# Optimization experiments

Hardware: AMD Instinct MI355X
Metric: run time of the kernel (lower is better)

## Reference

```python
import jax, jax.numpy as jnp
import numpy as np
from jax import lax

K_NN = 20          # cfg.nsample
BN_EPS = 1e-5


def fps(xyz, npoint, farthest0):
    """Furthest point sampling. xyz: [B,N,3] -> idx [B,npoint] (int)."""
    B, N, _ = xyz.shape

    def step(carry, _):
        distance, far = carry                                  # [B,N], [B]
        centroid = jnp.take_along_axis(xyz, far[:, None, None], axis=1)  # [B,1,3]
        d = jnp.sum((xyz - centroid) ** 2, axis=-1)            # [B,N]
        distance = jnp.minimum(distance, d)
        new_far = jnp.argmax(distance, axis=-1)
        return (distance, new_far), far

    init = (jnp.full((B, N), 1e10, dtype=xyz.dtype), farthest0)
    (_, _), idxs = lax.scan(step, init, None, length=npoint)   # idxs: [npoint,B]
    return jnp.transpose(idxs)                                 # [B,npoint]


def setup_inputs() -> dict:
    key = jax.random.key(0)
    k1, k2, k3, k4 = jax.random.split(key, 4)
    B, N, C = 4, 8192, 128
    c_in = C * 2 + 6   # mlps[0]*2 + 6 (use_xyz) = 262
    c_out = 256
    xyz = jax.random.normal(k1, (B, N, 3), dtype=jnp.float32)
    feat = jax.random.normal(k2, (B, N, C), dtype=jnp.float32)
    conv_w = jax.random.normal(k3, (c_in, c_out), dtype=jnp.float32) * 0.05  # 1x1 conv
    bn_gamma = jnp.ones((c_out,), dtype=jnp.float32)
    bn_beta = jnp.zeros((c_out,), dtype=jnp.float32)
    init_farthest = jax.random.randint(k4, (B,), 0, N)
    return {"xyz": xyz, "feat": feat, "conv_w": conv_w, "bn_gamma": bn_gamma,
            "bn_beta": bn_beta, "init_farthest": init_farthest, "npoints": 2048}


def reference(xyz, feat, conv_w, bn_gamma, bn_beta, init_farthest, npoints):
    # --- FPS sampling ---
    sample_idx = fps(xyz, npoints, init_farthest)                      # [B,S]
    new_xyz = jnp.take_along_axis(xyz, sample_idx[:, :, None], axis=1)  # [B,S,3]

    # --- augment features with xyz (use_xyz=True) ---
    feat_aug = jnp.concatenate([feat, xyz], axis=-1)                   # [B,N,131]
    new_feat_aug = jnp.take_along_axis(feat_aug, sample_idx[:, :, None], axis=1)  # [B,S,131]

    # --- KNN of new_xyz in xyz (squared L2, ascending) ---
    d2 = (jnp.sum(new_xyz ** 2, -1)[:, :, None]
          - 2.0 * jnp.einsum('bsd,bnd->bsn', new_xyz, xyz)
          + jnp.sum(xyz ** 2, -1)[:, None, :])                         # [B,S,N]
    _, knn_idx = lax.top_k(-d2, K_NN)                                  # [B,S,K]

    # --- gather neighbor features, build edge features ---
    knn_feat = jax.vmap(lambda f, i: f[i])(feat_aug, knn_idx)          # [B,S,K,131]
    center = new_feat_aug[:, :, None, :]                               # [B,S,1,131]
    edge = jnp.concatenate(
        [knn_feat - center, jnp.broadcast_to(center, knn_feat.shape)], axis=-1)  # [B,S,K,262]

    # --- shared MLP: 1x1 conv + BN (batch stats) + ReLU ---
    h = jnp.einsum('bskc,co->bsko', edge, conv_w)                      # [B,S,K,256]
    mean = jnp.mean(h, axis=(0, 1, 2))
    var = jnp.var(h, axis=(0, 1, 2))
    h = (h - mean) * lax.rsqrt(var + BN_EPS) * bn_gamma + bn_beta
    h = jax.nn.relu(h)

    # --- max-pool over K neighbors ---
    new_feat = jnp.max(h, axis=2)                                      # [B,S,256]
    return (new_xyz, new_feat, sample_idx)
```

## Files before the change

### kernel.cpp

```cpp
#include <hip/hip_runtime.h>
#include <hip/hip_bf16.h>


#define NPTS   8192
#define NSAMP  2048
#define KNN    20

typedef unsigned long long u64;
typedef unsigned int u32;
typedef unsigned short u16;

template<int CTRL, int RM>
__device__ __forceinline__ u64 dpp_kmax(u64 k) {
  unsigned lo = (unsigned)k, hi = (unsigned)(k >> 32);
  unsigned lo2 = (unsigned)__builtin_amdgcn_update_dpp((int)lo, (int)lo, CTRL, RM, 0xf, false);
  unsigned hi2 = (unsigned)__builtin_amdgcn_update_dpp((int)hi, (int)hi, CTRL, RM, 0xf, false);
  u64 o = ((u64)hi2 << 32) | lo2;
  return o > k ? o : k;
}
template<int CTRL, int RM>
__device__ __forceinline__ u64 dpp_kmin(u64 k) {
  unsigned lo = (unsigned)k, hi = (unsigned)(k >> 32);
  unsigned lo2 = (unsigned)__builtin_amdgcn_update_dpp((int)lo, (int)lo, CTRL, RM, 0xf, false);
  unsigned hi2 = (unsigned)__builtin_amdgcn_update_dpp((int)hi, (int)hi, CTRL, RM, 0xf, false);
  u64 o = ((u64)hi2 << 32) | lo2;
  return o < k ? o : k;
}
__device__ __forceinline__ u64 umax64(u64 a, u64 b) { return a > b ? a : b; }

__device__ __forceinline__ unsigned mspread4(unsigned q) {
  return (q & 1u) | ((q & 2u) << 2) | ((q & 4u) << 4) | ((q & 8u) << 6);
}

__global__ __launch_bounds__(1024, 1) void fps_kernel(
    const float* __restrict__ xyz, const int* __restrict__ farthest0,
    int* __restrict__ sample_int, float* __restrict__ out) {
  __shared__ float sxyz[NPTS * 3];
  __shared__ u16   sidxr[NPTS];
  __shared__ u32   s_samp[NSAMP];
  __shared__ u32   hist[4096];
  __shared__ u32   part[1024];
  __shared__ u64   slot[3];
  __shared__ int   s_isp;
  const int b = blockIdx.x, tid = threadIdx.x, lane = tid & 63;
  const float* xb = xyz + (size_t)b * NPTS * 3;

  for (int i = tid; i < 4096; i += 1024) hist[i] = 0u;
  if (tid < 3) slot[tid] = 0ull;
  __syncthreads();

  float ox[8], oy[8], oz[8];
  int cell[8];
#pragma unroll
  for (int j = 0; j < 8; ++j) {
    int p = tid * 8 + j;
    float x = xb[3*p], y = xb[3*p+1], z = xb[3*p+2];
    ox[j] = x; oy[j] = y; oz[j] = z;
    unsigned qx = (unsigned)(int)fminf(fmaxf((x + 5.2f) * 1.5384615f, 0.f), 15.f);
    unsigned qy = (unsigned)(int)fminf(fmaxf((y + 5.2f) * 1.5384615f, 0.f), 15.f);
    unsigned qz = (unsigned)(int)fminf(fmaxf((z + 5.2f) * 1.5384615f, 0.f), 15.f);
    cell[j] = (int)(mspread4(qx) | (mspread4(qy) << 1) | (mspread4(qz) << 2));
    atomicAdd(&hist[cell[j]], 1u);
  }
  __syncthreads();

  u32 h0 = hist[4*tid], h1 = hist[4*tid+1], h2 = hist[4*tid+2], h3 = hist[4*tid+3];
  u32 mysum = h0 + h1 + h2 + h3;
  part[tid] = mysum;
  __syncthreads();
  for (int off = 1; off < 1024; off <<= 1) {
    u32 u = (tid >= off) ? part[tid - off] : 0u;
    u32 v = part[tid];
    __syncthreads();
    part[tid] = u + v;
    __syncthreads();
  }
  u32 base = part[tid] - mysum;
  hist[4*tid]   = base;
  hist[4*tid+1] = base + h0;
  hist[4*tid+2] = base + h0 + h1;
  hist[4*tid+3] = base + h0 + h1 + h2;
  __syncthreads();

#pragma unroll
  for (int j = 0; j < 8; ++j) {
    u32 p = atomicAdd(&hist[cell[j]], 1u);
    sxyz[3*p] = ox[j]; sxyz[3*p+1] = oy[j]; sxyz[3*p+2] = oz[j];
    sidxr[p] = (u16)(tid * 8 + j);
  }
  __syncthreads();

  const int cur0 = farthest0[b];
#pragma unroll
  for (int j = 0; j < 8; ++j) {
    int p = tid * 8 + j;
    if ((int)sidxr[p] == cur0) s_isp = p;
  }

  float px[8], py[8], pz[8], dist[8];
  u32 low32[8];
#pragma unroll
  for (int j = 0; j < 8; ++j) {
    int p = tid * 8 + j;
    px[j] = sxyz[3*p]; py[j] = sxyz[3*p+1]; pz[j] = sxyz[3*p+2];
    low32[j] = (((~(u32)sidxr[p]) & 0x1FFFu) << 13) | (u32)p;
    dist[j] = 1e10f;
  }
  float lxmin = px[0], lxmax = px[0], lymin = py[0], lymax = py[0], lzmin = pz[0], lzmax = pz[0];
#pragma unroll
  for (int j = 1; j < 8; ++j) {
    lxmin = fminf(lxmin, px[j]); lxmax = fmaxf(lxmax, px[j]);
    lymin = fminf(lymin, py[j]); lymax = fmaxf(lymax, py[j]);
    lzmin = fminf(lzmin, pz[j]); lzmax = fmaxf(lzmax, pz[j]);
  }

  u64 klane = ((u64)__float_as_uint(1e10f) << 32);
  u64 kw    = ((u64)__float_as_uint(1e10f) << 32);
  __syncthreads();

  int cur_sp = s_isp;
  u32 cur_pack = ((u32)cur0 << 13) | (u32)cur_sp;

  for (int it = 0; it < NSAMP; ++it) {
    if (tid == 0) s_samp[it] = cur_pack;
    if (it == NSAMP - 1) break;
    if (tid == 64) slot[(it+2)%3] = 0ull;
    float3 c3 = *(const float3*)&sxyz[3*cur_sp];
    float cx = c3.x, cy = c3.y, cz = c3.z;

    float gx = fmaxf(fmaxf(__fsub_rn(lxmin, cx), __fsub_rn(cx, lxmax)), 0.f);
    float gy = fmaxf(fmaxf(__fsub_rn(lymin, cy), __fsub_rn(cy, lymax)), 0.f);
    float gz = fmaxf(fmaxf(__fsub_rn(lzmin, cz), __fsub_rn(cz, lzmax)), 0.f);
    float bound = __fadd_rn(__fadd_rn(__fmul_rn(gx,gx), __fmul_rn(gy,gy)), __fmul_rn(gz,gz));
    float ub = __uint_as_float((u32)(klane >> 32));
    bool live = !(__fmul_rn(bound, 0.999999f) >= ub);

    if (__any(live)) {
      if (live) {
#pragma unroll
        for (int j = 0; j < 8; ++j) {
          float dx = __fsub_rn(px[j], cx);
          float dy = __fsub_rn(py[j], cy);
          float dz = __fsub_rn(pz[j], cz);
          float d  = __fadd_rn(__fadd_rn(__fmul_rn(dx,dx), __fmul_rn(dy,dy)), __fmul_rn(dz,dz));
          dist[j] = fminf(dist[j], d);
        }
        u64 k0 = ((u64)__float_as_uint(dist[0]) << 32) | low32[0];
        u64 k1 = ((u64)__float_as_uint(dist[1]) << 32) | low32[1];
        u64 k2 = ((u64)__float_as_uint(dist[2]) << 32) | low32[2];
        u64 k3 = ((u64)__float_as_uint(dist[3]) << 32) | low32[3];
        u64 k4 = ((u64)__float_as_uint(dist[4]) << 32) | low32[4];
        u64 k5 = ((u64)__float_as_uint(dist[5]) << 32) | low32[5];
        u64 k6 = ((u64)__float_as_uint(dist[6]) << 32) | low32[6];
        u64 k7 = ((u64)__float_as_uint(dist[7]) << 32) | low32[7];
        klane = umax64(umax64(umax64(k0,k1), umax64(k2,k3)),
                       umax64(umax64(k4,k5), umax64(k6,k7)));
      }
      u64 k = klane;
      k = dpp_kmax<0xB1, 0xf>(k);
      k = dpp_kmax<0x4E, 0xf>(k);
      k = dpp_kmax<0x124, 0xf>(k);
      k = dpp_kmax<0x128, 0xf>(k);
      k = dpp_kmax<0x142, 0xa>(k);
      k = dpp_kmax<0x143, 0xc>(k);
      kw = k;
    }
    if (lane == 63) atomicMax(&slot[(it+1)%3], kw);
    __syncthreads();
    u64 wk = slot[(it+1)%3];
    u32 wlo = (u32)wk;
    cur_sp = (int)(wlo & 0x1FFFu);
    u32 org = (~(wlo >> 13)) & 0x1FFFu;
    cur_pack = (org << 13) | (u32)cur_sp;
  }

  __syncthreads();
  float* outxyz = out + (size_t)b * NSAMP * 3;
  float* outidx = out + 24576 + 2097152 + (size_t)b * NSAMP;
  for (int it = tid; it < NSAMP; it += 1024) {
    u32 s = s_samp[it];
    int org = (int)(s >> 13), sp = (int)(s & 0x1FFFu);
    sample_int[(b << 11) + it] = org;
    outidx[it] = (float)org;
    outxyz[3*it]   = sxyz[3*sp];
    outxyz[3*it+1] = sxyz[3*sp+1];
    outxyz[3*it+2] = sxyz[3*sp+2];
  }
}

__global__ __launch_bounds__(256, 1) void knn_kernel(
    const float* __restrict__ xyz, const int* __restrict__ sample_int,
    int* __restrict__ knn_out) {
  __shared__ u64 lists[2][2][KNN];
  const int tid  = threadIdx.x;
  const int lane = tid & 63, w = tid >> 6;
  const int ql   = w >> 1;
  const int ch   = w & 1;
  const int qq   = blockIdx.x * 2 + ql;
  const int b    = qq >> 11;
  const float* xb = xyz + (size_t)b * NPTS * 3;
  const int sidx = sample_int[qq];
  const float sx = xb[3*sidx], sy = xb[3*sidx+1], sz = xb[3*sidx+2];
  const float sqs = __fadd_rn(__fadd_rn(__fmul_rn(sx,sx), __fmul_rn(sy,sy)), __fmul_rn(sz,sz));

  const int pbase = ch * 4096;
  float d[64];
#pragma unroll
  for (int i = 0; i < 64; ++i) {
    int p = pbase + i*64 + lane;
    float x = xb[3*p], y = xb[3*p+1], z = xb[3*p+2];
    float dot = __fadd_rn(__fadd_rn(__fmul_rn(sx,x), __fmul_rn(sy,y)), __fmul_rn(sz,z));
    float sqx = __fadd_rn(__fadd_rn(__fmul_rn(x,x), __fmul_rn(y,y)), __fmul_rn(z,z));
    d[i] = __fadd_rn(__fsub_rn(sqs, __fmul_rn(2.0f, dot)), sqx);
  }
  u64 msk = 0ull;
  for (int kk = 0; kk < KNN; ++kk) {
    float bv = 1e30f; int bs = 0;
#pragma unroll
    for (int i = 0; i < 64; ++i) {
      float dc = (msk & (1ull << i)) ? 1e30f : d[i];
      if (dc < bv) { bv = dc; bs = i; }
    }
    unsigned gi = (unsigned)(pbase + bs*64 + lane);
    u64 key = ((u64)__float_as_uint(bv) << 32) | gi;
    key = dpp_kmin<0xB1, 0xf>(key);
    key = dpp_kmin<0x4E, 0xf>(key);
    key = dpp_kmin<0x124, 0xf>(key);
    key = dpp_kmin<0x128, 0xf>(key);
    key = dpp_kmin<0x142, 0xa>(key);
    key = dpp_kmin<0x143, 0xc>(key);
    unsigned glo = (unsigned)__builtin_amdgcn_readlane((int)(unsigned)key, 63);
    unsigned ghi = (unsigned)__builtin_amdgcn_readlane((int)(unsigned)(key >> 32), 63);
    if (lane == (int)(glo & 63u)) msk |= 1ull << ((glo - pbase) >> 6);
    if (lane == 0) lists[ql][ch][kk] = ((u64)ghi << 32) | glo;
  }
  __syncthreads();
  if (ch == 0) {
    u64 mykey = ~0ull; int rank = 64;
    if (lane < 40) {
      int li = lane >= 20 ? 1 : 0;
      int e  = li ? lane - 20 : lane;
      mykey = lists[ql][li][e];
      int cnt = e;
      const u64* oth = &lists[ql][li ^ 1][0];
#pragma unroll
      for (int j = 0; j < KNN; ++j) cnt += (oth[j] < mykey) ? 1 : 0;
      rank = cnt;
    }
    if (rank < KNN) knn_out[(size_t)qq * KNN + rank] = (int)(mykey & 0xFFFFFFFFull);
  }
}

__global__ void wdiff_kernel(const float* __restrict__ W, float* __restrict__ Wd) {
  int i = blockIdx.x * 256 + threadIdx.x;
  Wd[i] = W[131*256 + i] - W[i];
}

template<bool BF16OUT>
__global__ __launch_bounds__(128) void matmul131_kernel(
    const float* __restrict__ featb, const float* __restrict__ xyzb,
    const int* __restrict__ gidx,
    const float* __restrict__ W, void* __restrict__ outp) {
  __shared__ float tile[32][132];
  const int tid = threadIdx.x;
  const int r0  = blockIdx.x << 5;
  for (int i = tid; i < 32*131; i += 128) {
    int r = i / 131;
    int k = i - r*131;
    int row = r0 + r;
    int src;
    if (gidx) { int bb = row >> 11; src = (bb << 13) + gidx[row]; }
    else      { src = row; }
    float v = (k < 128) ? featb[(size_t)src*128 + k]
                        : xyzb[(size_t)src*3 + (k-128)];
    tile[r][k] = v;
  }
  __syncthreads();
  float acc0[32], acc1[32];
#pragma unroll
  for (int r = 0; r < 32; ++r) { acc0[r] = 0.f; acc1[r] = 0.f; }
  const int c0 = tid, c1 = tid + 128;
  for (int k = 0; k < 128; k += 4) {
    float w00 = W[(k+0)*256+c0], w01 = W[(k+1)*256+c0], w02 = W[(k+2)*256+c0], w03 = W[(k+3)*256+c0];
    float w10 = W[(k+0)*256+c1], w11 = W[(k+1)*256+c1], w12 = W[(k+2)*256+c1], w13 = W[(k+3)*256+c1];
#pragma unroll
    for (int r = 0; r < 32; ++r) {
      float4 a = *(const float4*)&tile[r][k];
      acc0[r] = fmaf(a.x, w00, acc0[r]); acc0[r] = fmaf(a.y, w01, acc0[r]);
      acc0[r] = fmaf(a.z, w02, acc0[r]); acc0[r] = fmaf(a.w, w03, acc0[r]);
      acc1[r] = fmaf(a.x, w10, acc1[r]); acc1[r] = fmaf(a.y, w11, acc1[r]);
      acc1[r] = fmaf(a.z, w12, acc1[r]); acc1[r] = fmaf(a.w, w13, acc1[r]);
    }
  }
#pragma unroll
  for (int kk = 128; kk < 131; ++kk) {
    float w0 = W[kk*256+c0], w1 = W[kk*256+c1];
#pragma unroll
    for (int r = 0; r < 32; ++r) {
      float a = tile[r][kk];
      acc0[r] = fmaf(a, w0, acc0[r]);
      acc1[r] = fmaf(a, w1, acc1[r]);
    }
  }
#pragma unroll
  for (int r = 0; r < 32; ++r) {
    if (BF16OUT) {
      __hip_bfloat16* o = (__hip_bfloat16*)outp;
      o[(size_t)(r0+r)*256 + c0] = __float2bfloat16(acc0[r]);
      o[(size_t)(r0+r)*256 + c1] = __float2bfloat16(acc1[r]);
    } else {
      float* o = (float*)outp;
      o[(size_t)(r0+r)*256 + c0] = acc0[r];
      o[(size_t)(r0+r)*256 + c1] = acc1[r];
    }
  }
}

__global__ __launch_bounds__(256) void stats_kernel(
    const __hip_bfloat16* __restrict__ Pb, const int* __restrict__ knn,
    float* __restrict__ outFeat, float* __restrict__ psum, float* __restrict__ psq,
    int qq0, int prow) {
  const int c = threadIdx.x;
  float s = 0.f, s2 = 0.f;
  const int q0 = qq0 + blockIdx.x * 16;
  for (int q = 0; q < 16; ++q) {
    int qq = q0 + q;
    float qc = outFeat[(size_t)qq*256 + c];
    float m = -1e30f;
    const int* kn = knn + (size_t)qq * KNN;
#pragma unroll
    for (int k = 0; k < KNN; ++k) {
      int idx = kn[k];
      float v = __bfloat162float(Pb[(size_t)idx*256 + c]) + qc;
      m = fmaxf(m, v);
      s += v;
      s2 = fmaf(v, v, s2);
    }
    outFeat[(size_t)qq*256 + c] = m;
  }
  psum[(size_t)(prow + blockIdx.x)*256 + c] = s;
  psq [(size_t)(prow + blockIdx.x)*256 + c] = s2;
}

__global__ __launch_bounds__(256) void stats_all_kernel(
    const __hip_bfloat16* __restrict__ Pall,
    const int* __restrict__ knn, float* __restrict__ outFeat,
    float* __restrict__ psum, float* __restrict__ psq) {
  const int c = threadIdx.x;
  float s = 0.f, s2 = 0.f;
  const int q0 = blockIdx.x * 16;
  for (int q = 0; q < 16; ++q) {
    int qq = q0 + q;
    int b = qq >> 11;
    const __hip_bfloat16* Pb = Pall + (size_t)b * NPTS * 256;
    float qc = outFeat[(size_t)qq*256 + c];
    float m = -1e30f;
    const int* kn = knn + (size_t)qq * KNN;
#pragma unroll
    for (int k = 0; k < KNN; ++k) {
      int idx = kn[k];
      float v = __bfloat162float(Pb[(size_t)idx*256 + c]) + qc;
      m = fmaxf(m, v);
      s += v;
      s2 = fmaf(v, v, s2);
    }
    outFeat[(size_t)qq*256 + c] = m;
  }
  psum[(size_t)blockIdx.x*256 + c] = s;
  psq [(size_t)blockIdx.x*256 + c] = s2;
}

__global__ __launch_bounds__(256) void reduce_stats_kernel(
    const float* __restrict__ psum, const float* __restrict__ psq,
    const float* __restrict__ gamma, const float* __restrict__ beta,
    float* __restrict__ ss) {
  const int c = blockIdx.x, t = threadIdx.x;
  float s  = psum[(size_t)t*256 + c] + psum[(size_t)(t+256)*256 + c];
  float s2 = psq [(size_t)t*256 + c] + psq [(size_t)(t+256)*256 + c];
#pragma unroll
  for (int off = 32; off >= 1; off >>= 1) {
    s  += __shfl_xor(s,  off);
    s2 += __shfl_xor(s2, off);
  }
  __shared__ float as[4], as2[4];
  const int lane = t & 63, wid = t >> 6;
  if (lane == 0) { as[wid] = s; as2[wid] = s2; }
  __syncthreads();
  if (t == 0) {
    float S  = (as[0]+as[1]) + (as[2]+as[3]);
    float S2 = (as2[0]+as2[1]) + (as2[2]+as2[3]);
    const float inv = 1.f / 163840.f;
    float mean = S * inv;
    float var  = S2 * inv - mean * mean;
    float sc = rsqrtf(var + 1e-5f) * gamma[c];
    ss[c]       = sc;
    ss[256 + c] = beta[c] - mean * sc;
  }
}

__global__ __launch_bounds__(256) void finalize_kernel(
    float* __restrict__ f, const float* __restrict__ ss) {
  int e = blockIdx.x * 256 + threadIdx.x;
  float v = fmaf(f[e], ss[threadIdx.x], ss[256 + threadIdx.x]);
  f[e] = v > 0.f ? v : 0.f;
}

extern "C" void kernel_launch(void* const* d_in, const int* in_sizes, int n_in,
                              void* d_out, int out_size, void* d_ws, size_t ws_size,
                              hipStream_t stream) {
  const float* xyz      = (const float*)d_in[0];
  const float* feat     = (const float*)d_in[1];
  const float* conv_w   = (const float*)d_in[2];
  const float* bn_gamma = (const float*)d_in[3];
  const float* bn_beta  = (const float*)d_in[4];
  const int*   far0     = (const int*)d_in[5];

  char* ws = (char*)d_ws;
  int*   sample_int = (int*)  (ws + 0);
  int*   knn        = (int*)  (ws + 32768);
  float* Wd         = (float*)(ws + 688128);
  float* psum       = (float*)(ws + 822272);
  float* psq        = (float*)(ws + 1346560);
  float* ss         = (float*)(ws + 1870848);
  __hip_bfloat16* Pb = (__hip_bfloat16*)(ws + 2097152);

  float* out     = (float*)d_out;
  float* outFeat = out + 24576;

  const bool fused = ws_size >= (size_t)(2097152 + 33554432/2);

  fps_kernel  <<<dim3(4),    dim3(1024), 0, stream>>>(xyz, far0, sample_int, out);
  knn_kernel  <<<dim3(4096), dim3(256),  0, stream>>>(xyz, sample_int, knn);
  wdiff_kernel<<<dim3(131),  dim3(256),  0, stream>>>(conv_w, Wd);

  matmul131_kernel<false><<<dim3(256), dim3(128), 0, stream>>>(
      feat, xyz, sample_int, Wd, (void*)outFeat);

  if (fused) {
    matmul131_kernel<true><<<dim3(1024), dim3(128), 0, stream>>>(
        feat, xyz, (const int*)nullptr, conv_w, (void*)Pb);
    stats_all_kernel<<<dim3(512), dim3(256), 0, stream>>>(
        Pb, knn, outFeat, psum, psq);
  } else {
    for (int b = 0; b < 4; ++b) {
      matmul131_kernel<true><<<dim3(256), dim3(128), 0, stream>>>(
          feat + (size_t)b*NPTS*128, xyz + (size_t)b*NPTS*3,
          (const int*)nullptr, conv_w, (void*)Pb);
      stats_kernel<<<dim3(128), dim3(256), 0, stream>>>(
          Pb, knn + (size_t)b*NSAMP*KNN, outFeat + (size_t)b*NSAMP*256,
          psum, psq, 0, b*128);
    }
  }

  reduce_stats_kernel<<<dim3(256), dim3(256), 0, stream>>>(psum, psq, bn_gamma, bn_beta, ss);
  finalize_kernel   <<<dim3(8192), dim3(256), 0, stream>>>(outFeat, ss);
}
```

Measured before the change: 1.918 ms.

## Halve FPS block size and replace shared atomicMax with per-wave slot reduction

Measured after the change: 2.852 ms. 48.7% more time.

```diff
diff --git a/kernel.cpp b/kernel.cpp
--- a/kernel.cpp
+++ b/kernel.cpp
@@ -32,28 +32,27 @@
   return (q & 1u) | ((q & 2u) << 2) | ((q & 4u) << 4) | ((q & 8u) << 6);
 }
 
-__global__ __launch_bounds__(1024, 1) void fps_kernel(
+__global__ __launch_bounds__(512, 1) void fps_kernel(
     const float* __restrict__ xyz, const int* __restrict__ farthest0,
     int* __restrict__ sample_int, float* __restrict__ out) {
   __shared__ float sxyz[NPTS * 3];
   __shared__ u16   sidxr[NPTS];
   __shared__ u32   s_samp[NSAMP];
   __shared__ u32   hist[4096];
-  __shared__ u32   part[1024];
-  __shared__ u64   slot[3];
+  __shared__ u32   part[512];
+  __shared__ u64   skey[2][8];
   __shared__ int   s_isp;
-  const int b = blockIdx.x, tid = threadIdx.x, lane = tid & 63;
+  const int b = blockIdx.x, tid = threadIdx.x, lane = tid & 63, wid = tid >> 6;
   const float* xb = xyz + (size_t)b * NPTS * 3;
 
-  for (int i = tid; i < 4096; i += 1024) hist[i] = 0u;
-  if (tid < 3) slot[tid] = 0ull;
-  __syncthreads();
-
-  float ox[8], oy[8], oz[8];
-  int cell[8];
-#pragma unroll
-  for (int j = 0; j < 8; ++j) {
-    int p = tid * 8 + j;
+  for (int i = tid; i < 4096; i += 512) hist[i] = 0u;
+  __syncthreads();
+
+  float ox[16], oy[16], oz[16];
+  int cell[16];
+#pragma unroll
+  for (int j = 0; j < 16; ++j) {
+    int p = tid * 16 + j;
     float x = xb[3*p], y = xb[3*p+1], z = xb[3*p+2];
     ox[j] = x; oy[j] = y; oz[j] = z;
     unsigned qx = (unsigned)(int)fminf(fmaxf((x + 5.2f) * 1.5384615f, 0.f), 15.f);
@@ -64,11 +63,12 @@
   }
   __syncthreads();
 
-  u32 h0 = hist[4*tid], h1 = hist[4*tid+1], h2 = hist[4*tid+2], h3 = hist[4*tid+3];
-  u32 mysum = h0 + h1 + h2 + h3;
+  u32 h[8]; u32 mysum = 0u;
+#pragma unroll
+  for (int j = 0; j < 8; ++j) { h[j] = hist[8*tid + j]; mysum += h[j]; }
   part[tid] = mysum;
   __syncthreads();
-  for (int off = 1; off < 1024; off <<= 1) {
+  for (int off = 1; off < 512; off <<= 1) {
     u32 u = (tid >= off) ? part[tid - off] : 0u;
     u32 v = part[tid];
     __syncthreads();
@@ -76,39 +76,37 @@
     __syncthreads();
   }
   u32 base = part[tid] - mysum;
-  hist[4*tid]   = base;
-  hist[4*tid+1] = base + h0;
-  hist[4*tid+2] = base + h0 + h1;
-  hist[4*tid+3] = base + h0 + h1 + h2;
-  __syncthreads();
-
-#pragma unroll
-  for (int j = 0; j < 8; ++j) {
+#pragma unroll
+  for (int j = 0; j < 8; ++j) { u32 nb = base + h[j]; hist[8*tid + j] = base; base = nb; }
+  __syncthreads();
+
+#pragma unroll
+  for (int j = 0; j < 16; ++j) {
     u32 p = atomicAdd(&hist[cell[j]], 1u);
     sxyz[3*p] = ox[j]; sxyz[3*p+1] = oy[j]; sxyz[3*p+2] = oz[j];
-    sidxr[p] = (u16)(tid * 8 + j);
+    sidxr[p] = (u16)(tid * 16 + j);
   }
   __syncthreads();
 
   const int cur0 = farthest0[b];
 #pragma unroll
-  for (int j = 0; j < 8; ++j) {
-    int p = tid * 8 + j;
+  for (int j = 0; j < 16; ++j) {
+    int p = tid * 16 + j;
     if ((int)sidxr[p] == cur0) s_isp = p;
   }
 
-  float px[8], py[8], pz[8], dist[8];
-  u32 low32[8];
-#pragma unroll
-  for (int j = 0; j < 8; ++j) {
-    int p = tid * 8 + j;
+  float px[16], py[16], pz[16], dist[16];
+  u32 low32[16];
+#pragma unroll
+  for (int j = 0; j < 16; ++j) {
+    int p = tid * 16 + j;
     px[j] = sxyz[3*p]; py[j] = sxyz[3*p+1]; pz[j] = sxyz[3*p+2];
     low32[j] = (((~(u32)sidxr[p]) & 0x1FFFu) << 13) | (u32)p;
     dist[j] = 1e10f;
   }
   float lxmin = px[0], lxmax = px[0], lymin = py[0], lymax = py[0], lzmin = pz[0], lzmax = pz[0];
 #pragma unroll
-  for (int j = 1; j < 8; ++j) {
+  for (int j = 1; j < 16; ++j) {
     lxmin = fminf(lxmin, px[j]); lxmax = fmaxf(lxmax, px[j]);
     lymin = fminf(lymin, py[j]); lymax = fmaxf(lymax, py[j]);
     lzmin = fminf(lzmin, pz[j]); lzmax = fmaxf(lzmax, pz[j]);
@@ -124,7 +122,6 @@
   for (int it = 0; it < NSAMP; ++it) {
     if (tid == 0) s_samp[it] = cur_pack;
     if (it == NSAMP - 1) break;
-    if (tid == 64) slot[(it+2)%3] = 0ull;
     float3 c3 = *(const float3*)&sxyz[3*cur_sp];
     float cx = c3.x, cy = c3.y, cz = c3.z;
 
@@ -137,24 +134,18 @@
 
     if (__any(live)) {
       if (live) {
-#pragma unroll
-        for (int j = 0; j < 8; ++j) {
+        u64 kacc = 0ull;
+#pragma unroll
+        for (int j = 0; j < 16; ++j) {
           float dx = __fsub_rn(px[j], cx);
           float dy = __fsub_rn(py[j], cy);
           float dz = __fsub_rn(pz[j], cz);
           float d  = __fadd_rn(__fadd_rn(__fmul_rn(dx,dx), __fmul_rn(dy,dy)), __fmul_rn(dz,dz));
-          dist[j] = fminf(dist[j], d);
+          float dd = fminf(dist[j], d);
+          dist[j] = dd;
+          kacc = umax64(kacc, ((u64)__float_as_uint(dd) << 32) | low32[j]);
         }
-        u64 k0 = ((u64)__float_as_uint(dist[0]) << 32) | low32[0];
-        u64 k1 = ((u64)__float_as_uint(dist[1]) << 32) | low32[1];
-        u64 k2 = ((u64)__float_as_uint(dist[2]) << 32) | low32[2];
-        u64 k3 = ((u64)__float_as_uint(dist[3]) << 32) | low32[3];
-        u64 k4 = ((u64)__float_as_uint(dist[4]) << 32) | low32[4];
-        u64 k5 = ((u64)__float_as_uint(dist[5]) << 32) | low32[5];
-        u64 k6 = ((u64)__float_as_uint(dist[6]) << 32) | low32[6];
-        u64 k7 = ((u64)__float_as_uint(dist[7]) << 32) | low32[7];
-        klane = umax64(umax64(umax64(k0,k1), umax64(k2,k3)),
-                       umax64(umax64(k4,k5), umax64(k6,k7)));
+        klane = kacc;
       }
       u64 k = klane;
       k = dpp_kmax<0xB1, 0xf>(k);
@@ -165,9 +156,12 @@
       k = dpp_kmax<0x143, 0xc>(k);
       kw = k;
     }
-    if (lane == 63) atomicMax(&slot[(it+1)%3], kw);
+    if (lane == 63) skey[it & 1][wid] = kw;
     __syncthreads();
-    u64 wk = slot[(it+1)%3];
+    u64 wk = skey[it & 1][lane & 7];
+    wk = dpp_kmax<0xB1, 0xf>(wk);
+    wk = dpp_kmax<0x4E, 0xf>(wk);
+    wk = dpp_kmax<0x124, 0xf>(wk);
     u32 wlo = (u32)wk;
     cur_sp = (int)(wlo & 0x1FFFu);
     u32 org = (~(wlo >> 13)) & 0x1FFFu;
@@ -177,7 +171,7 @@
   __syncthreads();
   float* outxyz = out + (size_t)b * NSAMP * 3;
   float* outidx = out + 24576 + 2097152 + (size_t)b * NSAMP;
-  for (int it = tid; it < NSAMP; it += 1024) {
+  for (int it = tid; it < NSAMP; it += 512) {
     u32 s = s_samp[it];
     int org = (int)(s >> 13), sp = (int)(s & 0x1FFFu);
     sample_int[(b << 11) + it] = org;
@@ -429,7 +423,7 @@
 
   const bool fused = ws_size >= (size_t)(2097152 + 33554432/2);
 
-  fps_kernel  <<<dim3(4),    dim3(1024), 0, stream>>>(xyz, far0, sample_int, out);
+  fps_kernel  <<<dim3(4),    dim3(512),  0, stream>>>(xyz, far0, sample_int, out);
   knn_kernel  <<<dim3(4096), dim3(256),  0, stream>>>(xyz, sample_int, knn);
   wdiff_kernel<<<dim3(131),  dim3(256),  0, stream>>>(conv_w, Wd);
 
```

## Overlap FPS with dense matmul and weight-diff in one merged kernel launch

Applied to the files above, without the earlier changes.

Result: slower. 1.999 ms (+4.2%).

```diff
diff --git a/kernel.cpp b/kernel.cpp
--- a/kernel.cpp
+++ b/kernel.cpp
@@ -26,23 +26,105 @@
   u64 o = ((u64)hi2 << 32) | lo2;
   return o < k ? o : k;
 }
+template<int CTRL, int RM>
+__device__ __forceinline__ float dpp_fmax(float x) {
+  int t = __builtin_amdgcn_update_dpp(__float_as_int(x), __float_as_int(x), CTRL, RM, 0xf, false);
+  return fmaxf(x, __int_as_float(t));
+}
+template<int CTRL, int RM>
+__device__ __forceinline__ float dpp_fmin(float x) {
+  int t = __builtin_amdgcn_update_dpp(__float_as_int(x), __float_as_int(x), CTRL, RM, 0xf, false);
+  return fminf(x, __int_as_float(t));
+}
 __device__ __forceinline__ u64 umax64(u64 a, u64 b) { return a > b ? a : b; }
+
+__device__ __forceinline__ float wave_fmax_bcast(float x) {
+  x = dpp_fmax<0xB1, 0xf>(x); x = dpp_fmax<0x4E, 0xf>(x);
+  x = dpp_fmax<0x124, 0xf>(x); x = dpp_fmax<0x128, 0xf>(x);
+  x = dpp_fmax<0x142, 0xa>(x); x = dpp_fmax<0x143, 0xc>(x);
+  return __int_as_float(__builtin_amdgcn_readlane(__float_as_int(x), 63));
+}
+__device__ __forceinline__ float wave_fmin_bcast(float x) {
+  x = dpp_fmin<0xB1, 0xf>(x); x = dpp_fmin<0x4E, 0xf>(x);
+  x = dpp_fmin<0x124, 0xf>(x); x = dpp_fmin<0x128, 0xf>(x);
+  x = dpp_fmin<0x142, 0xa>(x); x = dpp_fmin<0x143, 0xc>(x);
+  return __int_as_float(__builtin_amdgcn_readlane(__float_as_int(x), 63));
+}
 
 __device__ __forceinline__ unsigned mspread4(unsigned q) {
   return (q & 1u) | ((q & 2u) << 2) | ((q & 4u) << 4) | ((q & 8u) << 6);
 }
 
-__global__ __launch_bounds__(1024, 1) void fps_kernel(
+#define NM_BLOCKS 128
+__global__ __launch_bounds__(1024, 1) void mega_kernel(
     const float* __restrict__ xyz, const int* __restrict__ farthest0,
-    int* __restrict__ sample_int, float* __restrict__ out) {
-  __shared__ float sxyz[NPTS * 3];
-  __shared__ u16   sidxr[NPTS];
-  __shared__ u32   s_samp[NSAMP];
-  __shared__ u32   hist[4096];
-  __shared__ u32   part[1024];
-  __shared__ u64   slot[3];
-  __shared__ int   s_isp;
-  const int b = blockIdx.x, tid = threadIdx.x, lane = tid & 63;
+    const float* __restrict__ feat, const float* __restrict__ conv_w,
+    int* __restrict__ sample_int, float* __restrict__ out,
+    __hip_bfloat16* __restrict__ Pb, float* __restrict__ Wd, int nmatmul) {
+  __shared__ u64 smem8[17984];
+  char* smem = (char*)smem8;
+  const int bid = blockIdx.x, tid = threadIdx.x;
+
+  if (bid >= 4) {
+    if (bid - 4 < nmatmul) {
+      float* tile = (float*)smem + (tid >> 7) * (32 * 132);
+      const int gtid = tid & 127;
+      const int r0 = (bid - 4) * 256 + (tid >> 7) * 32;
+      for (int i = gtid; i < 32 * 131; i += 128) {
+        int r = i / 131;
+        int k = i - r * 131;
+        int src = r0 + r;
+        float v = (k < 128) ? feat[(size_t)src * 128 + k]
+                            : xyz[(size_t)src * 3 + (k - 128)];
+        tile[r * 132 + k] = v;
+      }
+      __syncthreads();
+      float acc0[32], acc1[32];
+#pragma unroll
+      for (int r = 0; r < 32; ++r) { acc0[r] = 0.f; acc1[r] = 0.f; }
+      const int c0 = gtid, c1 = gtid + 128;
+      for (int k = 0; k < 128; k += 4) {
+        float w00 = conv_w[(k+0)*256+c0], w01 = conv_w[(k+1)*256+c0], w02 = conv_w[(k+2)*256+c0], w03 = conv_w[(k+3)*256+c0];
+        float w10 = conv_w[(k+0)*256+c1], w11 = conv_w[(k+1)*256+c1], w12 = conv_w[(k+2)*256+c1], w13 = conv_w[(k+3)*256+c1];
+#pragma unroll
+        for (int r = 0; r < 32; ++r) {
+          float4 a = *(const float4*)&tile[r * 132 + k];
+          acc0[r] = fmaf(a.x, w00, acc0[r]); acc0[r] = fmaf(a.y, w01, acc0[r]);
+          acc0[r] = fmaf(a.z, w02, acc0[r]); acc0[r] = fmaf(a.w, w03, acc0[r]);
+          acc1[r] = fmaf(a.x, w10, acc1[r]); acc1[r] = fmaf(a.y, w11, acc1[r]);
+          acc1[r] = fmaf(a.z, w12, acc1[r]); acc1[r] = fmaf(a.w, w13, acc1[r]);
+        }
+      }
+#pragma unroll
+      for (int kk = 128; kk < 131; ++kk) {
+        float w0 = conv_w[kk*256+c0], w1 = conv_w[kk*256+c1];
+#pragma unroll
+        for (int r = 0; r < 32; ++r) {
+          float a = tile[r * 132 + kk];
+          acc0[r] = fmaf(a, w0, acc0[r]);
+          acc1[r] = fmaf(a, w1, acc1[r]);
+        }
+      }
+#pragma unroll
+      for (int r = 0; r < 32; ++r) {
+        Pb[(size_t)(r0 + r) * 256 + c0] = __float2bfloat16(acc0[r]);
+        Pb[(size_t)(r0 + r) * 256 + c1] = __float2bfloat16(acc1[r]);
+      }
+    } else {
+      int i = (bid - 4 - nmatmul) * 1024 + tid;
+      if (i < 131 * 256) Wd[i] = conv_w[131 * 256 + i] - conv_w[i];
+    }
+    return;
+  }
+
+  float* sxyz  = (float*)smem;
+  u16*   sidxr = (u16*)(smem + 98304);
+  u32*   s_samp= (u32*)(smem + 114688);
+  u32*   hist  = (u32*)(smem + 122880);
+  u32*   part  = (u32*)(smem + 139264);
+  u64*   slot  = (u64*)(smem + 143360);
+  int*   s_isp = (int*)(smem + 143384);
+  const int b = bid, lane = tid & 63;
   const float* xb = xyz + (size_t)b * NPTS * 3;
 
   for (int i = tid; i < 4096; i += 1024) hist[i] = 0u;
@@ -94,7 +176,7 @@
 #pragma unroll
   for (int j = 0; j < 8; ++j) {
     int p = tid * 8 + j;
-    if ((int)sidxr[p] == cur0) s_isp = p;
+    if ((int)sidxr[p] == cur0) *s_isp = p;
   }
 
   float px[8], py[8], pz[8], dist[8];
@@ -113,12 +195,15 @@
     lymin = fminf(lymin, py[j]); lymax = fmaxf(lymax, py[j]);
     lzmin = fminf(lzmin, pz[j]); lzmax = fmaxf(lzmax, pz[j]);
   }
+  const float wxmin = wave_fmin_bcast(lxmin), wxmax = wave_fmax_bcast(lxmax);
+  const float wymin = wave_fmin_bcast(lymin), wymax = wave_fmax_bcast(lymax);
+  const float wzmin = wave_fmin_bcast(lzmin), wzmax = wave_fmax_bcast(lzmax);
 
   u64 klane = ((u64)__float_as_uint(1e10f) << 32);
   u64 kw    = ((u64)__float_as_uint(1e10f) << 32);
   __syncthreads();
 
-  int cur_sp = s_isp;
+  int cur_sp = *s_isp;
   u32 cur_pack = ((u32)cur0 << 13) | (u32)cur_sp;
 
   for (int it = 0; it < NSAMP; ++it) {
@@ -128,42 +213,49 @@
     float3 c3 = *(const float3*)&sxyz[3*cur_sp];
     float cx = c3.x, cy = c3.y, cz = c3.z;
 
-    float gx = fmaxf(fmaxf(__fsub_rn(lxmin, cx), __fsub_rn(cx, lxmax)), 0.f);
-    float gy = fmaxf(fmaxf(__fsub_rn(lymin, cy), __fsub_rn(cy, lymax)), 0.f);
-    float gz = fmaxf(fmaxf(__fsub_rn(lzmin, cz), __fsub_rn(cz, lzmax)), 0.f);
-    float bound = __fadd_rn(__fadd_rn(__fmul_rn(gx,gx), __fmul_rn(gy,gy)), __fmul_rn(gz,gz));
-    float ub = __uint_as_float((u32)(klane >> 32));
-    bool live = !(__fmul_rn(bound, 0.999999f) >= ub);
-
-    if (__any(live)) {
-      if (live) {
-#pragma unroll
-        for (int j = 0; j < 8; ++j) {
-          float dx = __fsub_rn(px[j], cx);
-          float dy = __fsub_rn(py[j], cy);
-          float dz = __fsub_rn(pz[j], cz);
-          float d  = __fadd_rn(__fadd_rn(__fmul_rn(dx,dx), __fmul_rn(dy,dy)), __fmul_rn(dz,dz));
-          dist[j] = fminf(dist[j], d);
+    float wgx = fmaxf(fmaxf(__fsub_rn(wxmin, cx), __fsub_rn(cx, wxmax)), 0.f);
+    float wgy = fmaxf(fmaxf(__fsub_rn(wymin, cy), __fsub_rn(cy, wymax)), 0.f);
+    float wgz = fmaxf(fmaxf(__fsub_rn(wzmin, cz), __fsub_rn(cz, wzmax)), 0.f);
+    float wbound = __fadd_rn(__fadd_rn(__fmul_rn(wgx,wgx), __fmul_rn(wgy,wgy)), __fmul_rn(wgz,wgz));
+    float ubw = __int_as_float(__builtin_amdgcn_readlane((int)(u32)(kw >> 32), 63));
+    if (!(__fmul_rn(wbound, 0.999999f) >= ubw)) {
+      float gx = fmaxf(fmaxf(__fsub_rn(lxmin, cx), __fsub_rn(cx, lxmax)), 0.f);
+      float gy = fmaxf(fmaxf(__fsub_rn(lymin, cy), __fsub_rn(cy, lymax)), 0.f);
+      float gz = fmaxf(fmaxf(__fsub_rn(lzmin, cz), __fsub_rn(cz, lzmax)), 0.f);
+      float bound = __fadd_rn(__fadd_rn(__fmul_rn(gx,gx), __fmul_rn(gy,gy)), __fmul_rn(gz,gz));
+      float ub = __uint_as_float((u32)(klane >> 32));
+      bool live = !(__fmul_rn(bound, 0.999999f) >= ub);
+
+      if (__any(live)) {
+        if (live) {
+#pragma unroll
+          for (int j = 0; j < 8; ++j) {
+            float dx = __fsub_rn(px[j], cx);
+            float dy = __fsub_rn(py[j], cy);
+            float dz = __fsub_rn(pz[j], cz);
+            float d  = __fadd_rn(__fadd_rn(__fmul_rn(dx,dx), __fmul_rn(dy,dy)), __fmul_rn(dz,dz));
+            dist[j] = fminf(dist[j], d);
+          }
+          u64 k0 = ((u64)__float_as_uint(dist[0]) << 32) | low32[0];
+          u64 k1 = ((u64)__float_as_uint(dist[1]) << 32) | low32[1];
+          u64 k2 = ((u64)__float_as_uint(dist[2]) << 32) | low32[2];
+          u64 k3 = ((u64)__float_as_uint(dist[3]) << 32) | low32[3];
+          u64 k4 = ((u64)__float_as_uint(dist[4]) << 32) | low32[4];
+          u64 k5 = ((u64)__float_as_uint(dist[5]) << 32) | low32[5];
+          u64 k6 = ((u64)__float_as_uint(dist[6]) << 32) | low32[6];
+          u64 k7 = ((u64)__float_as_uint(dist[7]) << 32) | low32[7];
+          klane = umax64(umax64(umax64(k0,k1), umax64(k2,k3)),
+                         umax64(umax64(k4,k5), umax64(k6,k7)));
         }
-        u64 k0 = ((u64)__float_as_uint(dist[0]) << 32) | low32[0];
-        u64 k1 = ((u64)__float_as_uint(dist[1]) << 32) | low32[1];
-        u64 k2 = ((u64)__float_as_uint(dist[2]) << 32) | low32[2];
-        u64 k3 = ((u64)__float_as_uint(dist[3]) << 32) | low32[3];
-        u64 k4 = ((u64)__float_as_uint(dist[4]) << 32) | low32[4];
-        u64 k5 = ((u64)__float_as_uint(dist[5]) << 32) | low32[5];
-        u64 k6 = ((u64)__float_as_uint(dist[6]) << 32) | low32[6];
-        u64 k7 = ((u64)__float_as_uint(dist[7]) << 32) | low32[7];
-        klane = umax64(umax64(umax64(k0,k1), umax64(k2,k3)),
-                       umax64(umax64(k4,k5), umax64(k6,k7)));
+        u64 k = klane;
+        k = dpp_kmax<0xB1, 0xf>(k);
+        k = dpp_kmax<0x4E, 0xf>(k);
+        k = dpp_kmax<0x124, 0xf>(k);
+        k = dpp_kmax<0x128, 0xf>(k);
+        k = dpp_kmax<0x142, 0xa>(k);
+        k = dpp_kmax<0x143, 0xc>(k);
+        kw = k;
       }
-      u64 k = klane;
-      k = dpp_kmax<0xB1, 0xf>(k);
-      k = dpp_kmax<0x4E, 0xf>(k);
-      k = dpp_kmax<0x124, 0xf>(k);
-      k = dpp_kmax<0x128, 0xf>(k);
-      k = dpp_kmax<0x142, 0xa>(k);
-      k = dpp_kmax<0x143, 0xc>(k);
-      kw = k;
     }
     if (lane == 63) atomicMax(&slot[(it+1)%3], kw);
     __syncthreads();
@@ -249,11 +341,6 @@
     }
     if (rank < KNN) knn_out[(size_t)qq * KNN + rank] = (int)(mykey & 0xFFFFFFFFull);
   }
-}
-
-__global__ void wdiff_kernel(const float* __restrict__ W, float* __restrict__ Wd) {
-  int i = blockIdx.x * 256 + threadIdx.x;
-  Wd[i] = W[131*256 + i] - W[i];
 }
 
 template<bool BF16OUT>
@@ -316,6 +403,11 @@
   }
 }
 
+__global__ void wdiff_kernel(const float* __restrict__ W, float* __restrict__ Wd) {
+  int i = blockIdx.x * 256 + threadIdx.x;
+  Wd[i] = W[131*256 + i] - W[i];
+}
+
 __global__ __launch_bounds__(256) void stats_kernel(
     const __hip_bfloat16* __restrict__ Pb, const int* __restrict__ knn,
     float* __restrict__ outFeat, float* __restrict__ psum, float* __restrict__ psq,
@@ -429,19 +521,20 @@
 
   const bool fused = ws_size >= (size_t)(2097152 + 33554432/2);
 
-  fps_kernel  <<<dim3(4),    dim3(1024), 0, stream>>>(xyz, far0, sample_int, out);
-  knn_kernel  <<<dim3(4096), dim3(256),  0, stream>>>(xyz, sample_int, knn);
-  wdiff_kernel<<<dim3(131),  dim3(256),  0, stream>>>(conv_w, Wd);
-
-  matmul131_kernel<false><<<dim3(256), dim3(128), 0, stream>>>(
-      feat, xyz, sample_int, Wd, (void*)outFeat);
-
   if (fused) {
-    matmul131_kernel<true><<<dim3(1024), dim3(128), 0, stream>>>(
-        feat, xyz, (const int*)nullptr, conv_w, (void*)Pb);
+    mega_kernel<<<dim3(4 + NM_BLOCKS + 33), dim3(1024), 0, stream>>>(
+        xyz, far0, feat, conv_w, sample_int, out, Pb, Wd, NM_BLOCKS);
+    knn_kernel<<<dim3(4096), dim3(256), 0, stream>>>(xyz, sample_int, knn);
+    matmul131_kernel<false><<<dim3(256), dim3(128), 0, stream>>>(
+        feat, xyz, sample_int, Wd, (void*)outFeat);
     stats_all_kernel<<<dim3(512), dim3(256), 0, stream>>>(
         Pb, knn, outFeat, psum, psq);
   } else {
+    mega_kernel<<<dim3(4 + 33), dim3(1024), 0, stream>>>(
+        xyz, far0, feat, conv_w, sample_int, out, Pb, Wd, 0);
+    knn_kernel<<<dim3(4096), dim3(256), 0, stream>>>(xyz, sample_int, knn);
+    matmul131_kernel<false><<<dim3(256), dim3(128), 0, stream>>>(
+        feat, xyz, sample_int, Wd, (void*)outFeat);
     for (int b = 0; b < 4; ++b) {
       matmul131_kernel<true><<<dim3(256), dim3(128), 0, stream>>>(
           feat + (size_t)b*NPTS*128, xyz + (size_t)b*NPTS*3,
```
